# Kernel optimization log

Hardware: AMD Instinct MI355X
Metric: run time of the kernel (lower is better)

## Reference

```python
import jax, jax.numpy as jnp
import numpy as np

B = 1024   # batch
N = 512    # points per sample (fixed by Linear(512,128))
G = 32     # voxel grid side (fixed: 5 stride-2 convs must reach 1^3)
CH = [1, 4, 16, 32, 64, 128]
BN_EPS = 1e-5


def _basis():
    # PointEmbed sinusoidal basis: hidden_dim=48 -> 8 freqs per axis, [3, 24]
    e = (2.0 ** np.arange(8)).astype(np.float32) * np.pi
    z = np.zeros(8, np.float32)
    b = np.stack([np.concatenate([e, z, z]),
                  np.concatenate([z, e, z]),
                  np.concatenate([z, z, e])])
    return jnp.asarray(b)


def setup_inputs() -> dict:
    key = jax.random.key(0)
    ks = jax.random.split(key, 16)
    inp = {
        "voxels": jax.random.normal(ks[0], (B, 1, G, G, G), jnp.float32),
        "centers": jax.random.uniform(ks[1], (B, N, 3), jnp.float32) * 2.0 - 1.0,
    }
    for i in range(5):
        cin, cout = CH[i], CH[i + 1]
        inp[f"W{i+1}"] = jax.random.normal(ks[2 + i], (cout, cin, 3, 3, 3), jnp.float32) * 0.05
        inp[f"b{i+1}"] = jnp.zeros((cout,), jnp.float32)
        inp[f"g{i+1}"] = jnp.ones((cout,), jnp.float32)
        inp[f"beta{i+1}"] = jnp.zeros((cout,), jnp.float32)
    inp["pe_w"] = jax.random.normal(ks[7], (51, 128), jnp.float32) * 0.05  # Linear(48+3, 128)
    inp["pe_b"] = jnp.zeros((128,), jnp.float32)
    inp["f1_w"] = jax.random.normal(ks[8], (128, 1), jnp.float32) * 0.05   # ff_128_1
    inp["f1_b"] = jnp.zeros((1,), jnp.float32)
    inp["f2_w"] = jax.random.normal(ks[9], (512, 128), jnp.float32) * 0.05  # ff_512_128
    inp["f2_b"] = jnp.zeros((128,), jnp.float32)
    return inp


def _conv_bn_relu(x, W, b, g, beta):
    # SparseConv3d(k=3, s=2, p=1) on fully-occupied grid == dense conv; BN in batch-stats mode
    y = jax.lax.conv_general_dilated(
        x, W, window_strides=(2, 2, 2), padding=[(1, 1)] * 3,
        dimension_numbers=("NCDHW", "OIDHW", "NCDHW"))
    y = y + b[None, :, None, None, None]
    m = jnp.mean(y, axis=(0, 2, 3, 4), keepdims=True)
    v = jnp.var(y, axis=(0, 2, 3, 4), keepdims=True)
    y = (y - m) * jax.lax.rsqrt(v + BN_EPS)
    y = y * g[None, :, None, None, None] + beta[None, :, None, None, None]
    return jax.nn.relu(y)


def reference(voxels, centers,
              W1, b1, g1, beta1, W2, b2, g2, beta2, W3, b3, g3, beta3,
              W4, b4, g4, beta4, W5, b5, g5, beta5,
              pe_w, pe_b, f1_w, f1_b, f2_w, f2_b):
    # --- PointEmbed branch ---
    basis = _basis()                                      # [3, 24]
    proj = jnp.einsum("bnd,de->bne", centers, basis)      # [B, N, 24]
    emb = jnp.concatenate([jnp.sin(proj), jnp.cos(proj), centers], axis=2)  # [B, N, 51]
    xc = emb @ pe_w + pe_b                                # [B, N, 128]
    xc = (xc @ f1_w + f1_b)[..., 0]                       # [B, N=512]
    xc = xc @ f2_w + f2_b                                 # [B, 128]
    # --- sparse conv stack (dense-occupancy equivalent) ---
    x = voxels
    for W, b, g, be in ((W1, b1, g1, beta1), (W2, b2, g2, beta2),
                        (W3, b3, g3, beta3), (W4, b4, g4, beta4),
                        (W5, b5, g5, beta5)):
        x = _conv_bn_relu(x, W, b, g, be)
    x = x.reshape(-1, 128)                                # [B,128,1,1,1] -> [B,128]
    return x + xc
```

## Files before the change

### kernel.cpp

```cpp
#include <hip/hip_runtime.h>
#include <hip/hip_bf16.h>

#ifndef M_PI
#define M_PI 3.14159265358979323846
#endif

#define BN_EPS 1e-5f

#define OFF_Y1   0ull
#define OFF_Y2   16777216ull
#define OFF_Y3   25165824ull
#define OFF_Y4   27262976ull
#define OFF_Y5   27787264ull
#define OFF_S    27918336ull
#define OFF_W2G  28442624ull
#define OFF_W3G  28444352ull
#define OFF_W5G  28458176ull
#define OFF_U    28523712ull
#define OFF_SP1  28523776ull
#define OFF_SP2  28524288ull
#define OFF_SP3  28526336ull
#define OFF_SP4  28530432ull
#define OFF_SP5  28538624ull
#define SP_TOTAL 31232
#define OFF_W4G  OFF_Y1

__device__ __forceinline__ float wred(float v) {
    for (int m = 32; m; m >>= 1) v += __shfl_xor(v, m, 64);
    return v;
}

__device__ __forceinline__ void async_copy16(const void* g, void* l) {
    __builtin_amdgcn_global_load_lds((const __attribute__((address_space(1))) void*)g,
                                     (__attribute__((address_space(3))) void*)l,
                                     16, 0, 0);
}

__device__ __forceinline__ unsigned short f2bf(float f) {
    unsigned int x = __float_as_uint(f);
    unsigned int r = (x + 0x7fffu + ((x >> 16) & 1u)) >> 16;
    return (unsigned short)r;
}
__device__ __forceinline__ float bf2f(unsigned short u) {
    return __uint_as_float(((unsigned int)u) << 16);
}

__global__ void k_prep_w(const float* __restrict__ W2, const float* __restrict__ W3,
                         const float* __restrict__ W5,
                         float* __restrict__ w2g, float* __restrict__ w3g,
                         float* __restrict__ w5g, float* __restrict__ sp) {
    int idx = blockIdx.x * 256 + threadIdx.x;
    if (idx < 1728) {
        int co = idx & 15; int r = idx >> 4; int tap = r % 27; int ci = r / 27;
        w2g[idx] = W2[(co * 4 + ci) * 27 + tap];
        return;
    }
    idx -= 1728;
    if (idx < 13824) {
        int co = idx & 31; int r = idx >> 5; int tap = r % 27; int ci = r / 27;
        w3g[idx] = W3[(co * 16 + ci) * 27 + tap];
        return;
    }
    idx -= 13824;
    if (idx < 65536) {
        int co = idx & 127; int k = idx >> 7;
        int dx = k & 1, dy = (k >> 1) & 1, dz = (k >> 2) & 1, ci = k >> 3;
        w5g[idx] = W5[(co * 64 + ci) * 27 + (dz + 1) * 9 + (dy + 1) * 3 + (dx + 1)];
        return;
    }
    idx -= 65536;
    if (idx < SP_TOTAL) sp[idx] = 0.f;
}

__global__ void k_prep_w4(const float* __restrict__ W4, float* __restrict__ w4g) {
    int idx = blockIdx.x * 256 + threadIdx.x;
    if (idx < 55296) {
        int co = idx & 63; int r = idx >> 6;
        int tap = r % 27, ci = r / 27;
        w4g[idx] = W4[(co * 32 + ci) * 27 + tap];
    }
}

__global__ void k_prep_u(const float* __restrict__ pe_w, const float* __restrict__ pe_b,
                         const float* __restrict__ f1_w, const float* __restrict__ f1_b,
                         float* __restrict__ u) {
    int t = threadIdx.x;
    if (t < 51) {
        float acc = 0.f;
        for (int j = 0; j < 128; j++) acc += pe_w[t * 128 + j] * f1_w[j];
        u[t] = acc;
    } else if (t == 51) {
        float acc = f1_b[0];
        for (int j = 0; j < 128; j++) acc += pe_b[j] * f1_w[j];
        u[51] = acc;
    }
}

__global__ __launch_bounds__(256) void k_pe(const float* __restrict__ centers,
                                            const float* __restrict__ u,
                                            float* __restrict__ s) {
    __shared__ float us[52];
    int t = threadIdx.x;
    if (t < 52) us[t] = u[t];
    __syncthreads();
    int idx = blockIdx.x * 256 + t;
    float c3[3];
    c3[0] = centers[idx * 3 + 0];
    c3[1] = centers[idx * 3 + 1];
    c3[2] = centers[idx * 3 + 2];
    float acc = us[51] + c3[0] * us[48] + c3[1] * us[49] + c3[2] * us[50];
#pragma unroll
    for (int a = 0; a < 3; a++) {
#pragma unroll
        for (int f = 0; f < 8; f++) {
            float ang = c3[a] * (float)(M_PI * (double)(1 << f));
            float sv, cv;
            __sincosf(ang, &sv, &cv);
            acc += sv * us[a * 8 + f] + cv * us[24 + a * 8 + f];
        }
    }
    s[idx] = acc;
}

__global__ __launch_bounds__(256) void k_c1(const float* __restrict__ vox,
                                            const float* __restrict__ W1,
                                            const float* __restrict__ b1,
                                            unsigned short* __restrict__ y1b,
                                            float* __restrict__ sp1) {
    __shared__ __align__(16) float slab[9 * 1024];
    __shared__ __align__(16) float wl[112];
    __shared__ float red2[32];
    int bid = blockIdx.x;
    int b = bid >> 1, q = bid & 1;
    int t = threadIdx.x;
    const float* vb = vox + (size_t)b * 32768;
    int wu = __builtin_amdgcn_readfirstlane(t >> 6);

    if (t < 108) { int tap = t >> 2, co = t & 3; wl[t] = W1[co * 27 + tap]; }
    if (q == 0) ((float4*)slab)[t] = make_float4(0.f, 0.f, 0.f, 0.f);

    int p0 = 16 * q;
    int s0 = q ? 7 : 0;
    {
        int s = s0;
        for (int i = 0; i < 5; i++) {
            int p = p0 - 1 + i;
            if (p >= 0) async_copy16(vb + p * 1024 + t * 4, slab + s * 1024 + wu * 256);
            s++; if (s == 9) s = 0;
        }
    }
    int yo = t >> 4, xo = t & 15;
    int e = 2 * xo;
    int eA = (e >= 2) ? e - 2 : 0;
    float mx0 = xo ? 1.f : 0.f;
    int iyc[3]; float myv[3];
#pragma unroll
    for (int ky = 0; ky < 3; ky++) {
        int iy = 2 * yo + ky - 1;
        myv[ky] = (iy < 0) ? 0.f : 1.f;
        iyc[ky] = (iy < 0) ? 0 : iy;
    }
    float bb0 = b1[0], bb1 = b1[1], bb2 = b1[2], bb3 = b1[3];
    float sums[4] = {0.f, 0.f, 0.f, 0.f}, sqs[4] = {0.f, 0.f, 0.f, 0.f};

    asm volatile("s_waitcnt vmcnt(0)" ::: "memory");
    __syncthreads();

    int s_win = s0;
    for (int j = 0; j < 4; j++) {
        int zq = 4 * q + j;
        if (j < 3) {
            int sp = s_win + 5; if (sp >= 9) sp -= 9;
            for (int i = 0; i < 4; i++) {
                int p = 4 * zq + 4 + i;
                async_copy16(vb + p * 1024 + t * 4, slab + sp * 1024 + wu * 256);
                sp++; if (sp == 9) sp = 0;
            }
        }
        int P[5];
        {
            int s = s_win;
#pragma unroll
            for (int i = 0; i < 5; i++) { P[i] = s * 1024; s++; if (s == 9) s = 0; }
        }
        float a0[4] = {bb0, bb1, bb2, bb3};
        float a1[4] = {bb0, bb1, bb2, bb3};
#pragma unroll
        for (int kz = 0; kz < 3; kz++) {
            const float* pz0 = slab + P[kz];
            const float* pz1 = slab + P[kz + 2];
#pragma unroll
            for (int ky = 0; ky < 3; ky++) {
                int ro = iyc[ky] * 32;
                float2 xa0 = *(const float2*)(pz0 + ro + eA);
                float2 xb0 = *(const float2*)(pz0 + ro + e);
                float2 xa1 = *(const float2*)(pz1 + ro + eA);
                float2 xb1 = *(const float2*)(pz1 + ro + e);
                float m1 = myv[ky], m0 = m1 * mx0;
                const float* wt = wl + (kz * 9 + ky * 3) * 4;
                float4 w0 = *(const float4*)(wt);
                float4 w1 = *(const float4*)(wt + 4);
                float4 w2 = *(const float4*)(wt + 8);
                float v00 = xa0.y * m0, v01 = xb0.x * m1, v02 = xb0.y * m1;
                float v10 = xa1.y * m0, v11 = xb1.x * m1, v12 = xb1.y * m1;
                a0[0] += v00 * w0.x + v01 * w1.x + v02 * w2.x;
                a0[1] += v00 * w0.y + v01 * w1.y + v02 * w2.y;
                a0[2] += v00 * w0.z + v01 * w1.z + v02 * w2.z;
                a0[3] += v00 * w0.w + v01 * w1.w + v02 * w2.w;
                a1[0] += v10 * w0.x + v11 * w1.x + v12 * w2.x;
                a1[1] += v10 * w0.y + v11 * w1.y + v12 * w2.y;
                a1[2] += v10 * w0.z + v11 * w1.z + v12 * w2.z;
                a1[3] += v10 * w0.w + v11 * w1.w + v12 * w2.w;
            }
        }
        size_t base = (size_t)b * 16384 + (size_t)(2 * zq) * 256 + t;
#pragma unroll
        for (int c = 0; c < 4; c++) {
            y1b[base + c * 4096] = f2bf(a0[c]);
            y1b[base + c * 4096 + 256] = f2bf(a1[c]);
            sums[c] += a0[c] + a1[c];
            sqs[c] += a0[c] * a0[c] + a1[c] * a1[c];
        }
        s_win += 4; if (s_win >= 9) s_win -= 9;
        asm volatile("s_waitcnt vmcnt(0)" ::: "memory");
        __syncthreads();
    }
    int lane = t & 63, w = t >> 6;
#pragma unroll
    for (int c = 0; c < 4; c++) { sums[c] = wred(sums[c]); sqs[c] = wred(sqs[c]); }
    if (lane == 0) {
#pragma unroll
        for (int c = 0; c < 4; c++) { red2[w * 8 + c] = sums[c]; red2[w * 8 + 4 + c] = sqs[c]; }
    }
    __syncthreads();
    if (t < 8) {
        int c = t >> 1, isq = t & 1;
        float acc = red2[isq * 4 + c] + red2[8 + isq * 4 + c] +
                    red2[16 + isq * 4 + c] + red2[24 + isq * 4 + c];
        atomicAdd(&sp1[(2 * c + isq) * 64 + (bid & 63)], acc);
    }
}

__global__ __launch_bounds__(256) void k_c2(const unsigned short* __restrict__ y1b,
                                            const float* __restrict__ w2g,
                                            const float* __restrict__ b2,
                                            const float* __restrict__ g1,
                                            const float* __restrict__ be1,
                                            const float* __restrict__ sp1,
                                            float* __restrict__ y2,
                                            float* __restrict__ sp2) {
    __shared__ __align__(16) unsigned short slab16[9216];
    __shared__ __align__(16) float wl[1728];
    __shared__ float adl[8];
    __shared__ float red[8];
    int t = threadIdx.x;
    int bid = blockIdx.x;
    int b = bid >> 1, q = bid & 1;
    int w = t >> 6, lane = t & 63;
    int wu = __builtin_amdgcn_readfirstlane(w);
    const unsigned short* yb = y1b + (size_t)b * 16384;
    if (q == 0) ((float2*)slab16)[t] = make_float2(0.f, 0.f);
    {
        int h = wu & 1;
        int ci0 = h * 2 + (lane >> 5);
        int g = lane & 31;
        int gs = g ^ (((g >> 3) & 3) << 1);
        const unsigned short* src0 = yb + ci0 * 4096 + gs * 8;
        int pstart = wu >> 1;
        if (q == 0 && pstart == 0) pstart = 2;
        for (int p = pstart; p < 9; p += 2) {
            int zi = 8 * q - 1 + p;
            async_copy16(src0 + zi * 256, slab16 + p * 1024 + h * 512);
        }
    }
    for (int i = t; i < 1728; i += 256) wl[i] = w2g[i];
    for (int row = w; row < 8; row += 4) {
        float v = wred(sp1[row * 64 + lane]);
        if (lane == 0) red[row] = v;
    }
    __syncthreads();
    if (t < 4) {
        float cnt = 4194304.0f;
        float m = red[2 * t] / cnt;
        float var = red[2 * t + 1] / cnt - m * m;
        float a = g1[t] * rsqrtf(var + BN_EPS);
        adl[t] = a; adl[4 + t] = be1[t] - m * a;
    }
    asm volatile("s_waitcnt vmcnt(0)" ::: "memory");
    __syncthreads();
    int zp = w >> 1;
    int cgo = __builtin_amdgcn_readfirstlane((w & 1) * 8);
    int yo = lane >> 3, xo = lane & 7;
    float my0 = yo ? 1.f : 0.f, mx0 = xo ? 1.f : 0.f;
    float mzw = (q == 0 && zp == 0) ? 0.f : 1.f;
    int yw3[3], sw3[3], xh3[3], xp3[3];
#pragma unroll
    for (int k = 0; k < 3; k++) {
        int yi = 2 * yo + k - 1; int yc = yi < 0 ? 0 : yi;
        yw3[k] = yc * 8;
        sw3[k] = ((yc >> 2) & 3) << 3;
        int xi = 2 * xo + k - 1; int xv = xi < 0 ? 0 : xi;
        xh3[k] = xv >> 1; xp3[k] = xv & 1;
    }
    float aa[4], dd[4];
#pragma unroll
    for (int c = 0; c < 4; c++) { aa[c] = adl[c]; dd[c] = adl[4 + c]; }
    float acc0[8], acc1[8];
#pragma unroll
    for (int c = 0; c < 8; c++) { acc0[c] = b2[cgo + c]; acc1[c] = acc0[c]; }
    for (int ci = 0; ci < 4; ci++) {
        float a = aa[ci], d = dd[ci];
        const unsigned short* pb16 = slab16 + zp * 4096 + ci * 256;
        const float* wci = wl + ci * 432 + cgo;
#pragma unroll
        for (int kz = 0; kz < 3; kz++) {
            const unsigned short* pl = pb16 + kz * 1024;
#pragma unroll
            for (int ky = 0; ky < 3; ky++) {
                int wb = yw3[ky], sw = sw3[ky];
#pragma unroll
                for (int kx = 0; kx < 3; kx++) {
                    int idx = (((wb + xh3[kx]) ^ sw) << 1) | xp3[kx];
                    float v0 = bf2f(pl[idx]);
                    float v1 = bf2f(pl[idx + 2048]);
                    float vb0 = fmaxf(a * v0 + d, 0.f);
                    float vb1 = fmaxf(a * v1 + d, 0.f);
                    if (kz == 0) vb0 *= mzw;
                    if (ky == 0) { vb0 *= my0; vb1 *= my0; }
                    if (kx == 0) { vb0 *= mx0; vb1 *= mx0; }
                    const float* wt = wci + (kz * 9 + ky * 3 + kx) * 16;
                    float4 wA = *(const float4*)(wt);
                    float4 wB = *(const float4*)(wt + 4);
                    acc0[0] += vb0 * wA.x; acc0[1] += vb0 * wA.y;
                    acc0[2] += vb0 * wA.z; acc0[3] += vb0 * wA.w;
                    acc0[4] += vb0 * wB.x; acc0[5] += vb0 * wB.y;
                    acc0[6] += vb0 * wB.z; acc0[7] += vb0 * wB.w;
                    acc1[0] += vb1 * wA.x; acc1[1] += vb1 * wA.y;
                    acc1[2] += vb1 * wA.z; acc1[3] += vb1 * wA.w;
                    acc1[4] += vb1 * wB.x; acc1[5] += vb1 * wB.y;
                    acc1[6] += vb1 * wB.z; acc1[7] += vb1 * wB.w;
                }
            }
        }
    }
    int z0 = 4 * q + 2 * zp;
    size_t ob = (size_t)b * 8192 + (size_t)cgo * 512 + z0 * 64 + lane;
#pragma unroll
    for (int c = 0; c < 8; c++) {
        y2[ob + c * 512] = acc0[c];
        y2[ob + c * 512 + 64] = acc1[c];
    }
    int slot = bid & 63;
#pragma unroll
    for (int c = 0; c < 8; c++) {
        float s_ = wred(acc0[c] + acc1[c]);
        float q_ = wred(acc0[c] * acc0[c] + acc1[c] * acc1[c]);
        if (lane == 0) {
            atomicAdd(&sp2[(2 * (cgo + c)) * 64 + slot], s_);
            atomicAdd(&sp2[(2 * (cgo + c) + 1) * 64 + slot], q_);
        }
    }
}

__global__ __launch_bounds__(256) void k_c3(const float* __restrict__ y2,
                                            const float* __restrict__ w3g,
                                            const float* __restrict__ b3,
                                            const float* __restrict__ g2,
                                            const float* __restrict__ be2,
                                            const float* __restrict__ sp2,
                                            float* __restrict__ y3,
                                            float* __restrict__ sp3) {
    __shared__ __align__(16) float in3[8192];
    __shared__ float adl[32], red[32];
    int t = threadIdx.x;
    int b = blockIdx.x;
    int w = t >> 6, lane = t & 63;
    int wu = __builtin_amdgcn_readfirstlane(w);
    const float* yb = y2 + (size_t)b * 8192;
    for (int j = 0; j < 8; j++) {
        int s = ((j << 2) + (lane >> 4)) & 7;
        async_copy16(yb + wu * 2048 + j * 256 + ((lane ^ s) << 2),
                     in3 + wu * 2048 + j * 256);
    }
    for (int row = w; row < 32; row += 4) {
        float v = wred(sp2[row * 64 + lane]);
        if (lane == 0) red[row] = v;
    }
    __syncthreads();
    if (t < 16) {
        float cnt = 524288.0f;
        float m = red[2 * t] / cnt;
        float var = red[2 * t + 1] / cnt - m * m;
        float a = g2[t] * rsqrtf(var + BN_EPS);
        adl[t] = a; adl[16 + t] = be2[t] - m * a;
    }
    asm volatile("s_waitcnt vmcnt(0)" ::: "memory");
    __syncthreads();
    int px = lane & 3, py = (lane >> 2) & 3, pz = lane >> 4;
    float mz0 = pz ? 1.f : 0.f, my0 = py ? 1.f : 0.f, mx0 = px ? 1.f : 0.f;
    int zb3[3], sz3[3], yv3[3], xv3[3];
#pragma unroll
    for (int k = 0; k < 3; k++) {
        int zi = 2 * pz + k - 1; int zc = zi < 0 ? 0 : zi;
        zb3[k] = zc * 64; sz3[k] = zc << 2;
        int yi = 2 * py + k - 1; int yc = yi < 0 ? 0 : yi;
        yv3[k] = yc * 8;
        int xi = 2 * px + k - 1; xv3[k] = xi < 0 ? 0 : xi;
    }
    int coh = wu & 1, cih = wu >> 1;
    int cgo = coh * 16;
    float acc[16];
#pragma unroll
    for (int c = 0; c < 16; c++) acc[c] = 0.f;
    for (int cii = 0; cii < 8; cii++) {
        int ci = cih * 8 + cii;
        float a = adl[ci], d = adl[16 + ci];
        const float* base = in3 + ci * 512;
        const float* wci = w3g + ci * 864 + cgo;
#pragma unroll
        for (int kz = 0; kz < 3; kz++) {
            int A1 = zb3[kz], sz = sz3[kz];
#pragma unroll
            for (int ky = 0; ky < 3; ky++) {
                int A2 = A1 + yv3[ky];
#pragma unroll
                for (int kx = 0; kx < 3; kx++) {
                    float v = base[(A2 + xv3[kx]) ^ sz];
                    float vb = fmaxf(a * v + d, 0.f);
                    if (kz == 0) vb *= mz0;
                    if (ky == 0) vb *= my0;
                    if (kx == 0) vb *= mx0;
                    const float* wr = wci + (kz * 9 + ky * 3 + kx) * 32;
#pragma unroll
                    for (int c = 0; c < 16; c++) acc[c] += vb * wr[c];
                }
            }
        }
    }
    __syncthreads();
    if (wu >= 2) {
        float* pp = in3 + (wu & 1) * 1280 + lane * 20;
#pragma unroll
        for (int c4 = 0; c4 < 4; c4++)
            *(float4*)(pp + c4 * 4) = make_float4(acc[c4*4], acc[c4*4+1], acc[c4*4+2], acc[c4*4+3]);
    }
    __syncthreads();
    if (wu < 2) {
        const float* pp = in3 + wu * 1280 + lane * 20;
#pragma unroll
        for (int c = 0; c < 16; c++) acc[c] += pp[c] + b3[cgo + c];
        size_t ob = (size_t)b * 2048 + lane;
#pragma unroll
        for (int c = 0; c < 16; c++) y3[ob + (size_t)(cgo + c) * 64] = acc[c];
        int slot = b & 63;
#pragma unroll
        for (int c = 0; c < 16; c++) {
            float s_ = wred(acc[c]), q_ = wred(acc[c] * acc[c]);
            if (lane == 0) {
                atomicAdd(&sp3[(2 * (cgo + c)) * 64 + slot], s_);
                atomicAdd(&sp3[(2 * (cgo + c) + 1) * 64 + slot], q_);
            }
        }
    }
}

__global__ __launch_bounds__(256) void k_c4(const float* __restrict__ y3,
                                            const float* __restrict__ w4g,
                                            const float* __restrict__ b4,
                                            const float* __restrict__ g3,
                                            const float* __restrict__ be3,
                                            const float* __restrict__ sp3,
                                            float* __restrict__ y4,
                                            float* __restrict__ sp4) {
    __shared__ __align__(16) float in4[16416];
    __shared__ float adb[64], red[64];
    int t = threadIdx.x;
    int bid = blockIdx.x;
    int bq = bid >> 2, coq = bid & 3;
    int w = t >> 6, lane = t & 63;
    int wu = __builtin_amdgcn_readfirstlane(w);
#pragma unroll
    for (int h = 0; h < 2; h++) {
        int bs2 = wu * 2 + h;
        const float* src = y3 + (size_t)(bq * 8 + bs2) * 2048 + lane * 4;
        for (int j = 0; j < 8; j++)
            async_copy16(src + j * 256, in4 + bs2 * 2052 + j * 256);
    }
    for (int row = w; row < 64; row += 4) {
        float v = wred(sp3[row * 64 + lane]);
        if (lane == 0) red[row] = v;
    }
    __syncthreads();
    if (t < 32) {
        float cnt = 65536.0f;
        float m = red[2 * t] / cnt;
        float var = red[2 * t + 1] / cnt - m * m;
        float a = g3[t] * rsqrtf(var + BN_EPS);
        adb[t] = a; adb[32 + t] = be3[t] - m * a;
    }
    asm volatile("s_waitcnt vmcnt(0)" ::: "memory");
    __syncthreads();
    int bs = lane >> 3, pos = lane & 7;
    int pz = pos >> 2, py = (pos >> 1) & 1, px = pos & 1;
    int z0 = 2 * pz - 1; if (z0 < 0) z0 = 0;
    int y0 = 2 * py - 1; if (y0 < 0) y0 = 0;
    int x0 = 2 * px - 1; if (x0 < 0) x0 = 0;
    int zo_[3] = {z0 * 16, 2 * pz * 16, (2 * pz + 1) * 16};
    int yo_[3] = {y0 * 4, 2 * py * 4, (2 * py + 1) * 4};
    int xo_[3] = {x0, 2 * px, 2 * px + 1};
    float mz = pz ? 1.f : 0.f, my = py ? 1.f : 0.f, mx = px ? 1.f : 0.f;
    float acc[16];
#pragma unroll
    for (int c = 0; c < 16; c++) acc[c] = 0.f;
    const float* inb = in4 + bs * 2052;
    for (int cii = 0; cii < 8; cii++) {
        int ci = wu * 8 + cii;
        float a = adb[ci], d = adb[32 + ci];
        const float* inc = inb + ci * 64;
        const float* wcb = w4g + ci * 1728 + coq * 16;
#pragma unroll
        for (int kz = 0; kz < 3; kz++)
#pragma unroll
            for (int ky = 0; ky < 3; ky++)
#pragma unroll
                for (int kx = 0; kx < 3; kx++) {
                    float v = inc[zo_[kz] + yo_[ky] + xo_[kx]];
                    float vb = fmaxf(a * v + d, 0.f);
                    if (kz == 0) vb *= mz;
                    if (ky == 0) vb *= my;
                    if (kx == 0) vb *= mx;
                    const float* wr = wcb + (kz * 9 + ky * 3 + kx) * 64;
#pragma unroll
                    for (int c = 0; c < 16; c++) acc[c] += vb * wr[c];
                }
    }
    __syncthreads();
    if (wu > 0) {
        float* pp = in4 + (wu - 1) * 1280 + lane * 20;
#pragma unroll
        for (int c4 = 0; c4 < 4; c4++)
            *(float4*)(pp + c4 * 4) = make_float4(acc[c4*4], acc[c4*4+1], acc[c4*4+2], acc[c4*4+3]);
    }
    __syncthreads();
    if (wu == 0) {
#pragma unroll
        for (int p = 0; p < 3; p++) {
            const float* pp = in4 + p * 1280 + lane * 20;
#pragma unroll
            for (int c = 0; c < 16; c++) acc[c] += pp[c];
        }
        int bfull = bq * 8 + bs;
        size_t ob = (size_t)bfull * 512 + pos;
        int slot = bid & 63;
#pragma unroll
        for (int c = 0; c < 16; c++) {
            float vv = acc[c] + b4[coq * 16 + c];
            y4[ob + (size_t)(coq * 16 + c) * 8] = vv;
            acc[c] = vv;
        }
#pragma unroll
        for (int c = 0; c < 16; c++) {
            float s_ = wred(acc[c]), q_ = wred(acc[c] * acc[c]);
            if (lane == 0) {
                atomicAdd(&sp4[(2 * (coq * 16 + c)) * 64 + slot], s_);
                atomicAdd(&sp4[(2 * (coq * 16 + c) + 1) * 64 + slot], q_);
            }
        }
    }
}

__global__ __launch_bounds__(512) void k_c5(const float* __restrict__ y4,
                                            const float* __restrict__ w5g,
                                            const float* __restrict__ b5,
                                            const float* __restrict__ g4,
                                            const float* __restrict__ be4,
                                            const float* __restrict__ sp4,
                                            float* __restrict__ y5,
                                            float* __restrict__ sp5) {
    __shared__ __align__(16) float A[2048];
    __shared__ float P[512];
    __shared__ float ad[128], red[128];
    int t = threadIdx.x;
    int bq = blockIdx.x;
    int w = t >> 6, lane = t & 63;
    for (int row = w; row < 128; row += 8) {
        float v = wred(sp4[row * 64 + lane]);
        if (lane == 0) red[row] = v;
    }
    __syncthreads();
    if (t < 64) {
        float cnt = 8192.0f;
        float m = red[2 * t] / cnt;
        float var = red[2 * t + 1] / cnt - m * m;
        float a = g4[t] * rsqrtf(var + BN_EPS);
        ad[t] = a; ad[64 + t] = be4[t] - m * a;
    }
    __syncthreads();
    {
        int bs = t >> 7, k0 = (t & 127) << 2;
        float4 vv = *(const float4*)(y4 + (size_t)(bq * 4 + bs) * 512 + k0);
        int ci = k0 >> 3;
        float a = ad[ci], d = ad[64 + ci];
        float4 o;
        o.x = fmaxf(a * vv.x + d, 0.f);
        o.y = fmaxf(a * vv.y + d, 0.f);
        o.z = fmaxf(a * vv.z + d, 0.f);
        o.w = fmaxf(a * vv.w + d, 0.f);
        *(float4*)(A + bs * 512 + k0) = o;
    }
    __syncthreads();
    int bs = w & 3, kh = w >> 2;
    float acc0 = 0.f, acc1 = 0.f;
    const float* Ab = A + bs * 512 + kh * 256;
    const float* wp = w5g + kh * 32768 + lane * 2;
#pragma unroll 8
    for (int k = 0; k < 256; k++) {
        float2 wv = *(const float2*)(wp + k * 128);
        float av = Ab[k];
        acc0 += av * wv.x;
        acc1 += av * wv.y;
    }
    if (kh == 0) {
        P[bs * 128 + lane * 2] = acc0;
        P[bs * 128 + lane * 2 + 1] = acc1;
    }
    __syncthreads();
    if (kh == 1) {
        float f0 = acc0 + P[bs * 128 + lane * 2] + b5[lane * 2];
        float f1 = acc1 + P[bs * 128 + lane * 2 + 1] + b5[lane * 2 + 1];
        *(float2*)(y5 + (size_t)(bq * 4 + bs) * 128 + lane * 2) = make_float2(f0, f1);
        P[bs * 128 + lane * 2] = f0;
        P[bs * 128 + lane * 2 + 1] = f1;
    }
    __syncthreads();
    if (t < 128) {
        float s = 0.f, q = 0.f;
        for (int bb = 0; bb < 4; bb++) {
            float vv = P[bb * 128 + t];
            s += vv; q += vv * vv;
        }
        int slot = bq & 63;
        atomicAdd(&sp5[(2 * t) * 64 + slot], s);
        atomicAdd(&sp5[(2 * t + 1) * 64 + slot], q);
    }
}

__global__ __launch_bounds__(512) void k_f2(const float* __restrict__ s,
                                            const float* __restrict__ f2w,
                                            const float* __restrict__ f2b,
                                            const float* __restrict__ g5,
                                            const float* __restrict__ be5,
                                            const float* __restrict__ sp5,
                                            const float* __restrict__ y5,
                                            float* __restrict__ out) {
    __shared__ __align__(16) float A[2048];
    __shared__ float P[512];
    __shared__ float ad[256], red[256];
    int t = threadIdx.x;
    int bq = blockIdx.x;
    int w = t >> 6, lane = t & 63;
    for (int row = w; row < 256; row += 8) {
        float v = wred(sp5[row * 64 + lane]);
        if (lane == 0) red[row] = v;
    }
    __syncthreads();
    if (t < 128) {
        float cnt = 1024.0f;
        float m = red[2 * t] / cnt;
        float var = red[2 * t + 1] / cnt - m * m;
        float a = g5[t] * rsqrtf(var + BN_EPS);
        ad[t] = a; ad[128 + t] = be5[t] - m * a;
    }
    {
        int bs = t >> 7, k0 = (t & 127) << 2;
        float4 vv = *(const float4*)(s + (size_t)(bq * 4 + bs) * 512 + k0);
        *(float4*)(A + bs * 512 + k0) = vv;
    }
    __syncthreads();
    int bs = w & 3, kh = w >> 2;
    float acc0 = 0.f, acc1 = 0.f;
    const float* Ab = A + bs * 512 + kh * 256;
    const float* wp = f2w + kh * 32768 + lane * 2;
#pragma unroll 8
    for (int k = 0; k < 256; k++) {
        float2 wv = *(const float2*)(wp + k * 128);
        float av = Ab[k];
        acc0 += av * wv.x;
        acc1 += av * wv.y;
    }
    if (kh == 0) {
        P[bs * 128 + lane * 2] = acc0;
        P[bs * 128 + lane * 2 + 1] = acc1;
    }
    __syncthreads();
    if (kh == 1) {
        int b = bq * 4 + bs;
        int co = lane * 2;
        float2 vy = *(const float2*)(y5 + (size_t)b * 128 + co);
        float f0 = acc0 + P[bs * 128 + co] + f2b[co] +
                   fmaxf(ad[co] * vy.x + ad[128 + co], 0.f);
        float f1 = acc1 + P[bs * 128 + co + 1] + f2b[co + 1] +
                   fmaxf(ad[co + 1] * vy.y + ad[128 + co + 1], 0.f);
        *(float2*)(out + (size_t)b * 128 + co) = make_float2(f0, f1);
    }
}

extern "C" void kernel_launch(void* const* d_in, const int* in_sizes, int n_in,
                              void* d_out, int out_size, void* d_ws, size_t ws_size,
                              hipStream_t stream) {
    const float* vox     = (const float*)d_in[0];
    const float* centers = (const float*)d_in[1];
    const float* W1   = (const float*)d_in[2];
    const float* b1   = (const float*)d_in[3];
    const float* g1   = (const float*)d_in[4];
    const float* be1  = (const float*)d_in[5];
    const float* W2   = (const float*)d_in[6];
    const float* b2   = (const float*)d_in[7];
    const float* g2   = (const float*)d_in[8];
    const float* be2  = (const float*)d_in[9];
    const float* W3   = (const float*)d_in[10];
    const float* b3   = (const float*)d_in[11];
    const float* g3   = (const float*)d_in[12];
    const float* be3  = (const float*)d_in[13];
    const float* W4   = (const float*)d_in[14];
    const float* b4   = (const float*)d_in[15];
    const float* g4   = (const float*)d_in[16];
    const float* be4  = (const float*)d_in[17];
    const float* W5   = (const float*)d_in[18];
    const float* b5   = (const float*)d_in[19];
    const float* g5   = (const float*)d_in[20];
    const float* be5  = (const float*)d_in[21];
    const float* pe_w = (const float*)d_in[22];
    const float* pe_b = (const float*)d_in[23];
    const float* f1_w = (const float*)d_in[24];
    const float* f1_b = (const float*)d_in[25];
    const float* f2_w = (const float*)d_in[26];
    const float* f2_b = (const float*)d_in[27];

    float* ws  = (float*)d_ws;
    unsigned short* y1b = (unsigned short*)(ws + OFF_Y1);
    float* y2  = ws + OFF_Y2;
    float* y3  = ws + OFF_Y3;
    float* y4  = ws + OFF_Y4;
    float* y5  = ws + OFF_Y5;
    float* s   = ws + OFF_S;
    float* w2g = ws + OFF_W2G;
    float* w3g = ws + OFF_W3G;
    float* w4g = ws + OFF_W4G;
    float* w5g = ws + OFF_W5G;
    float* u   = ws + OFF_U;
    float* sp1 = ws + OFF_SP1;
    float* sp2 = ws + OFF_SP2;
    float* sp3 = ws + OFF_SP3;
    float* sp4 = ws + OFF_SP4;
    float* sp5 = ws + OFF_SP5;

    k_prep_w<<<439, 256, 0, stream>>>(W2, W3, W5, w2g, w3g, w5g, sp1);
    k_prep_u<<<1, 64, 0, stream>>>(pe_w, pe_b, f1_w, f1_b, u);
    k_pe<<<2048, 256, 0, stream>>>(centers, u, s);
    k_c1<<<2048, 256, 0, stream>>>(vox, W1, b1, y1b, sp1);
    k_c2<<<2048, 256, 0, stream>>>(y1b, w2g, b2, g1, be1, sp1, y2, sp2);
    k_prep_w4<<<216, 256, 0, stream>>>(W4, w4g);
    k_c3<<<1024, 256, 0, stream>>>(y2, w3g, b3, g2, be2, sp2, y3, sp3);
    k_c4<<<512, 256, 0, stream>>>(y3, w4g, b4, g3, be3, sp3, y4, sp4);
    k_c5<<<256, 512, 0, stream>>>(y4, w5g, b5, g4, be4, sp4, y5, sp5);
    k_f2<<<256, 512, 0, stream>>>(s, f2_w, f2_b, g5, be5, sp5, y5, (float*)d_out);
}
```

Before: 254.6 us.

## Split conv1 into per-wave z-planes and pre-apply BN1+ReLU in conv2 shared memory

Result: slower. 332.0 us (+30.4%).

```diff
diff --git a/kernel.cpp b/kernel.cpp
--- a/kernel.cpp
+++ b/kernel.cpp
@@ -127,117 +127,85 @@
                                             const float* __restrict__ b1,
                                             unsigned short* __restrict__ y1b,
                                             float* __restrict__ sp1) {
-    __shared__ __align__(16) float slab[9 * 1024];
+    __shared__ __align__(16) float slab[4][3072];
     __shared__ __align__(16) float wl[112];
-    __shared__ float red2[32];
+    int t = threadIdx.x, w = t >> 6, lane = t & 63;
+    int wu = __builtin_amdgcn_readfirstlane(w);
     int bid = blockIdx.x;
-    int b = bid >> 1, q = bid & 1;
-    int t = threadIdx.x;
+    int b = bid >> 2, zq = bid & 3;
+    int z = zq * 4 + wu;
     const float* vb = vox + (size_t)b * 32768;
-    int wu = __builtin_amdgcn_readfirstlane(t >> 6);
-
     if (t < 108) { int tap = t >> 2, co = t & 3; wl[t] = W1[co * 27 + tap]; }
-    if (q == 0) ((float4*)slab)[t] = make_float4(0.f, 0.f, 0.f, 0.f);
-
-    int p0 = 16 * q;
-    int s0 = q ? 7 : 0;
+    int pA = 2 * z - 1;
+    float mzA = (pA < 0) ? 0.f : 1.f;
+    if (pA < 0) pA = 0;
+    float* ls = slab[wu];
     {
-        int s = s0;
-        for (int i = 0; i < 5; i++) {
-            int p = p0 - 1 + i;
-            if (p >= 0) async_copy16(vb + p * 1024 + t * 4, slab + s * 1024 + wu * 256);
-            s++; if (s == 9) s = 0;
-        }
-    }
-    int yo = t >> 4, xo = t & 15;
-    int e = 2 * xo;
+        int pl0[3] = {pA, 2 * z, 2 * z + 1};
+#pragma unroll
+        for (int p = 0; p < 3; p++)
+#pragma unroll
+            for (int i = 0; i < 4; i++)
+                async_copy16(vb + pl0[p] * 1024 + i * 256 + lane * 4, ls + p * 1024 + i * 256);
+    }
+    asm volatile("s_waitcnt vmcnt(0)" ::: "memory");
+    __syncthreads();
+    int x = lane & 15, yo = lane >> 4;
+    int e = 2 * x;
     int eA = (e >= 2) ? e - 2 : 0;
-    float mx0 = xo ? 1.f : 0.f;
-    int iyc[3]; float myv[3];
-#pragma unroll
-    for (int ky = 0; ky < 3; ky++) {
-        int iy = 2 * yo + ky - 1;
-        myv[ky] = (iy < 0) ? 0.f : 1.f;
-        iyc[ky] = (iy < 0) ? 0 : iy;
-    }
+    float mx0 = x ? 1.f : 0.f;
     float bb0 = b1[0], bb1 = b1[1], bb2 = b1[2], bb3 = b1[3];
+    float acc[4][4];
+#pragma unroll
+    for (int k = 0; k < 4; k++) {
+        acc[k][0] = bb0; acc[k][1] = bb1; acc[k][2] = bb2; acc[k][3] = bb3;
+    }
+#pragma unroll
+    for (int kz = 0; kz < 3; kz++) {
+        const float* pz = ls + kz * 1024;
+        float mz = (kz == 0) ? mzA : 1.f;
+#pragma unroll
+        for (int ky = 0; ky < 3; ky++) {
+            int r0 = 2 * yo + ky - 1;
+            const float* wt = wl + (kz * 9 + ky * 3) * 4;
+            float4 w0 = *(const float4*)(wt);
+            float4 w1 = *(const float4*)(wt + 4);
+            float4 w2 = *(const float4*)(wt + 8);
+#pragma unroll
+            for (int k = 0; k < 4; k++) {
+                int r = r0 + 8 * k;
+                float mr = (r < 0) ? 0.f : mz;
+                int rc = (r < 0) ? 0 : r;
+                float2 xa = *(const float2*)(pz + rc * 32 + eA);
+                float2 xb = *(const float2*)(pz + rc * 32 + e);
+                float v0 = xa.y * (mr * mx0);
+                float v1 = xb.x * mr;
+                float v2 = xb.y * mr;
+                acc[k][0] += v0 * w0.x + v1 * w1.x + v2 * w2.x;
+                acc[k][1] += v0 * w0.y + v1 * w1.y + v2 * w2.y;
+                acc[k][2] += v0 * w0.z + v1 * w1.z + v2 * w2.z;
+                acc[k][3] += v0 * w0.w + v1 * w1.w + v2 * w2.w;
+            }
+        }
+    }
+    size_t base = (size_t)b * 16384 + (size_t)z * 256 + yo * 16 + x;
     float sums[4] = {0.f, 0.f, 0.f, 0.f}, sqs[4] = {0.f, 0.f, 0.f, 0.f};
-
-    asm volatile("s_waitcnt vmcnt(0)" ::: "memory");
-    __syncthreads();
-
-    int s_win = s0;
-    for (int j = 0; j < 4; j++) {
-        int zq = 4 * q + j;
-        if (j < 3) {
-            int sp = s_win + 5; if (sp >= 9) sp -= 9;
-            for (int i = 0; i < 4; i++) {
-                int p = 4 * zq + 4 + i;
-                async_copy16(vb + p * 1024 + t * 4, slab + sp * 1024 + wu * 256);
-                sp++; if (sp == 9) sp = 0;
-            }
-        }
-        int P[5];
-        {
-            int s = s_win;
-#pragma unroll
-            for (int i = 0; i < 5; i++) { P[i] = s * 1024; s++; if (s == 9) s = 0; }
-        }
-        float a0[4] = {bb0, bb1, bb2, bb3};
-        float a1[4] = {bb0, bb1, bb2, bb3};
-#pragma unroll
-        for (int kz = 0; kz < 3; kz++) {
-            const float* pz0 = slab + P[kz];
-            const float* pz1 = slab + P[kz + 2];
-#pragma unroll
-            for (int ky = 0; ky < 3; ky++) {
-                int ro = iyc[ky] * 32;
-                float2 xa0 = *(const float2*)(pz0 + ro + eA);
-                float2 xb0 = *(const float2*)(pz0 + ro + e);
-                float2 xa1 = *(const float2*)(pz1 + ro + eA);
-                float2 xb1 = *(const float2*)(pz1 + ro + e);
-                float m1 = myv[ky], m0 = m1 * mx0;
-                const float* wt = wl + (kz * 9 + ky * 3) * 4;
-                float4 w0 = *(const float4*)(wt);
-                float4 w1 = *(const float4*)(wt + 4);
-                float4 w2 = *(const float4*)(wt + 8);
-                float v00 = xa0.y * m0, v01 = xb0.x * m1, v02 = xb0.y * m1;
-                float v10 = xa1.y * m0, v11 = xb1.x * m1, v12 = xb1.y * m1;
-                a0[0] += v00 * w0.x + v01 * w1.x + v02 * w2.x;
-                a0[1] += v00 * w0.y + v01 * w1.y + v02 * w2.y;
-                a0[2] += v00 * w0.z + v01 * w1.z + v02 * w2.z;
-                a0[3] += v00 * w0.w + v01 * w1.w + v02 * w2.w;
-                a1[0] += v10 * w0.x + v11 * w1.x + v12 * w2.x;
-                a1[1] += v10 * w0.y + v11 * w1.y + v12 * w2.y;
-                a1[2] += v10 * w0.z + v11 * w1.z + v12 * w2.z;
-                a1[3] += v10 * w0.w + v11 * w1.w + v12 * w2.w;
-            }
-        }
-        size_t base = (size_t)b * 16384 + (size_t)(2 * zq) * 256 + t;
-#pragma unroll
-        for (int c = 0; c < 4; c++) {
-            y1b[base + c * 4096] = f2bf(a0[c]);
-            y1b[base + c * 4096 + 256] = f2bf(a1[c]);
-            sums[c] += a0[c] + a1[c];
-            sqs[c] += a0[c] * a0[c] + a1[c] * a1[c];
-        }
-        s_win += 4; if (s_win >= 9) s_win -= 9;
-        asm volatile("s_waitcnt vmcnt(0)" ::: "memory");
-        __syncthreads();
-    }
-    int lane = t & 63, w = t >> 6;
-#pragma unroll
-    for (int c = 0; c < 4; c++) { sums[c] = wred(sums[c]); sqs[c] = wred(sqs[c]); }
-    if (lane == 0) {
-#pragma unroll
-        for (int c = 0; c < 4; c++) { red2[w * 8 + c] = sums[c]; red2[w * 8 + 4 + c] = sqs[c]; }
-    }
-    __syncthreads();
-    if (t < 8) {
-        int c = t >> 1, isq = t & 1;
-        float acc = red2[isq * 4 + c] + red2[8 + isq * 4 + c] +
-                    red2[16 + isq * 4 + c] + red2[24 + isq * 4 + c];
-        atomicAdd(&sp1[(2 * c + isq) * 64 + (bid & 63)], acc);
+#pragma unroll
+    for (int c = 0; c < 4; c++)
+#pragma unroll
+        for (int k = 0; k < 4; k++) {
+            float v = acc[k][c];
+            y1b[base + c * 4096 + k * 64] = f2bf(v);
+            sums[c] += v; sqs[c] += v * v;
+        }
+    int slot = bid & 63;
+#pragma unroll
+    for (int c = 0; c < 4; c++) {
+        float s_ = wred(sums[c]), q_ = wred(sqs[c]);
+        if (lane == 0) {
+            atomicAdd(&sp1[(2 * c) * 64 + slot], s_);
+            atomicAdd(&sp1[(2 * c + 1) * 64 + slot], q_);
+        }
     }
 }
 
@@ -288,6 +256,18 @@
     }
     asm volatile("s_waitcnt vmcnt(0)" ::: "memory");
     __syncthreads();
+    {
+        unsigned int* s32 = (unsigned int*)slab16;
+        for (int j = t; j < 4608; j += 256) {
+            unsigned int v = s32[j];
+            int ci = (j >> 7) & 3;
+            float a = adl[ci], d = adl[4 + ci];
+            float lo = fmaxf(a * bf2f((unsigned short)(v & 0xffffu)) + d, 0.f);
+            float hi = fmaxf(a * bf2f((unsigned short)(v >> 16)) + d, 0.f);
+            s32[j] = ((unsigned int)f2bf(hi) << 16) | (unsigned int)f2bf(lo);
+        }
+    }
+    __syncthreads();
     int zp = w >> 1;
     int cgo = __builtin_amdgcn_readfirstlane((w & 1) * 8);
     int yo = lane >> 3, xo = lane & 7;
@@ -302,14 +282,10 @@
         int xi = 2 * xo + k - 1; int xv = xi < 0 ? 0 : xi;
         xh3[k] = xv >> 1; xp3[k] = xv & 1;
     }
-    float aa[4], dd[4];
-#pragma unroll
-    for (int c = 0; c < 4; c++) { aa[c] = adl[c]; dd[c] = adl[4 + c]; }
     float acc0[8], acc1[8];
 #pragma unroll
     for (int c = 0; c < 8; c++) { acc0[c] = b2[cgo + c]; acc1[c] = acc0[c]; }
     for (int ci = 0; ci < 4; ci++) {
-        float a = aa[ci], d = dd[ci];
         const unsigned short* pb16 = slab16 + zp * 4096 + ci * 256;
         const float* wci = wl + ci * 432 + cgo;
 #pragma unroll
@@ -321,10 +297,8 @@
 #pragma unroll
                 for (int kx = 0; kx < 3; kx++) {
                     int idx = (((wb + xh3[kx]) ^ sw) << 1) | xp3[kx];
-                    float v0 = bf2f(pl[idx]);
-                    float v1 = bf2f(pl[idx + 2048]);
-                    float vb0 = fmaxf(a * v0 + d, 0.f);
-                    float vb1 = fmaxf(a * v1 + d, 0.f);
+                    float vb0 = bf2f(pl[idx]);
+                    float vb1 = bf2f(pl[idx + 2048]);
                     if (kz == 0) vb0 *= mzw;
                     if (ky == 0) { vb0 *= my0; vb1 *= my0; }
                     if (kx == 0) { vb0 *= mx0; vb1 *= mx0; }
@@ -758,7 +732,7 @@
     k_prep_w<<<439, 256, 0, stream>>>(W2, W3, W5, w2g, w3g, w5g, sp1);
     k_prep_u<<<1, 64, 0, stream>>>(pe_w, pe_b, f1_w, f1_b, u);
     k_pe<<<2048, 256, 0, stream>>>(centers, u, s);
-    k_c1<<<2048, 256, 0, stream>>>(vox, W1, b1, y1b, sp1);
+    k_c1<<<4096, 256, 0, stream>>>(vox, W1, b1, y1b, sp1);
     k_c2<<<2048, 256, 0, stream>>>(y1b, w2g, b2, g1, be1, sp1, y2, sp2);
     k_prep_w4<<<216, 256, 0, stream>>>(W4, w4g);
     k_c3<<<1024, 256, 0, stream>>>(y2, w3g, b3, g2, be2, sp2, y3, sp3);
```
